# Kernel tuning notes

Measured on AMD Instinct MI355X. Metric: run time of the kernel, lower is better.

The kernel has to match this reference:

```python
import jax, jax.numpy as jnp
import numpy as np
jax.config.update("jax_enable_x64", True)

T_OLD = 60000
T_NEW = 60000
NV = 30000
MAX_STEPS = 300
FB_CHUNK = 500  # T_OLD must be divisible by this

FACE_OPP = np.array([[1, 2, 3], [0, 2, 3], [0, 1, 3], [0, 1, 2]])
EDGES = [(0, 1), (0, 2), (0, 3), (1, 2), (1, 3), (2, 3)]


def setup_inputs() -> dict:
    key = jax.random.key(0)
    k1, k2, k3, k4, k5 = jax.random.split(key, 5)
    # distinct vertices per tet (sorted base + strictly increasing offsets)
    off = jnp.arange(4, dtype=jnp.int64)
    new_indices = jnp.sort(jax.random.randint(k1, (T_NEW, 4), 0, NV - 4, dtype=jnp.int64), axis=1) + off
    old_indices = jnp.sort(jax.random.randint(k2, (T_OLD, 4), 0, NV - 4, dtype=jnp.int64), axis=1) + off
    return {
        "new_indices": new_indices,
        "old_indices": old_indices,
        "old_cc": jax.random.normal(k3, (T_OLD, 3), dtype=jnp.float32),
        "new_cc": jax.random.normal(k4, (T_NEW, 3), dtype=jnp.float32),
        "vertex_positions": jax.random.uniform(k5, (NV, 3), dtype=jnp.float32),
    }


def _min_edge_length(verts, indices):
    p = verts[indices]  # (T,4,3)
    el = jnp.stack([jnp.linalg.norm(p[:, a] - p[:, b], axis=-1) for a, b in EDGES])
    return el.min(axis=0)


def _forward(new_indices, old_indices, old_cc, new_cc, vertex_positions):
    T_new = new_indices.shape[0]
    T_old = old_indices.shape[0]
    Vn = vertex_positions.shape[0]

    # --- 1. unchanged-tet detection via sorted-vertex int64 keys ---
    key4 = lambda s: ((s[:, 0] * Vn + s[:, 1]) * Vn + s[:, 2]) * Vn + s[:, 3]
    ok = key4(jnp.sort(old_indices, axis=1))
    nk = key4(jnp.sort(new_indices, axis=1))
    order = jnp.argsort(ok)
    sk = ok[order]
    pos = jnp.searchsorted(sk, nk, side='right') - 1
    posc = jnp.clip(pos, 0, T_old - 1)
    matched = jnp.where((pos >= 0) & (sk[posc] == nk), order[posc], -1)
    is_matched = matched >= 0
    matched_safe = jnp.maximum(matched, 0)

    # --- 2. face adjacency of old mesh (sorted face keys, adjacent-equal pairing) ---
    fi = jnp.sort(old_indices[:, FACE_OPP], axis=2)          # (T_old,4,3)
    fk = (fi[..., 0] * Vn + fi[..., 1]) * Vn + fi[..., 2]    # (T_old,4)
    all_keys = fk.T.reshape(-1)                              # f-major like the numpy concat
    all_tets = jnp.tile(jnp.arange(T_old), 4)
    all_locals = jnp.repeat(jnp.arange(4), T_old)
    o2 = jnp.argsort(all_keys)
    sk2, st, sl = all_keys[o2], all_tets[o2], all_locals[o2]
    same = sk2[:-1] == sk2[1:]
    neighbors = jnp.full((T_old, 4), -1, dtype=jnp.int64)
    neighbors = neighbors.at[jnp.where(same, st[:-1], T_old), sl[:-1]].set(st[1:], mode='drop')
    neighbors = neighbors.at[jnp.where(same, st[1:], T_old), sl[1:]].set(st[:-1], mode='drop')

    # --- 3. per-old-tet inverse edge matrix; degenerate tets get no neighbors ---
    verts = jax.lax.stop_gradient(vertex_positions).astype(jnp.float32)
    p = verts[old_indices]                                   # (T_old,4,3)
    v0 = p[:, 0]
    Tm = jnp.stack([p[:, 1] - v0, p[:, 2] - v0, p[:, 3] - v0], axis=-1)
    degen = jnp.abs(jnp.linalg.det(Tm)) < 1e-10
    Tinv = jnp.linalg.inv(jnp.where(degen[:, None, None], jnp.eye(3, dtype=Tm.dtype), Tm))
    neighbors = jnp.where(degen[:, None], -1, neighbors)

    prio = jnp.full((Vn,), -1, dtype=jnp.int64)
    ar = jnp.arange(T_old)
    for vi in range(4):
        prio = prio.at[old_indices[:, vi]].max(vi * T_old + ar)
    v2t = jnp.where(prio >= 0, prio % T_old, 0)

    # --- 5. barycentric walk (masked, all float inputs stop-gradiented; int outputs) ---
    cent = jax.lax.stop_gradient(verts[new_indices].mean(axis=1))  # (T_new,3)
    seed = v2t[new_indices[:, 0]]
    n_walk = jnp.sum(~is_matched)
    thr = jnp.maximum(jnp.int64(100), n_walk // 1000)

    def cond(state):
        step, cur, rem, act = state
        return (step < MAX_STEPS) & (jnp.sum(act) >= thr)

    def body(state):
        step, cur, rem, act = state
        rel = cent - v0[cur]
        bary = jnp.einsum('nij,nj->ni', Tinv[cur], rel)
        all_b = jnp.concatenate([(1.0 - bary.sum(axis=1))[:, None], bary], axis=1)
        conv = act & (all_b.min(axis=1) >= -1e-4)
        rem = jnp.where(conv, cur, rem)
        act = act & ~conv
        nb = neighbors[cur, jnp.argmin(all_b, axis=1)]
        at_bd = act & (nb < 0)
        rem = jnp.where(at_bd, cur, rem)
        act = act & ~at_bd
        cur = jnp.where(act, nb, cur)
        return (step + 1, cur, rem, act)

    _, cur, rem, act = jax.lax.while_loop(cond, body, (jnp.int64(0), seed, seed, ~is_matched))
    rem = jnp.where(act, cur, rem)

    # --- 6. nearest-centroid fallback for unfinished walks (gated, chunked) ---
    old_cents = jax.lax.stop_gradient(verts[old_indices].mean(axis=1))

    def fallback(_):
        p2 = (cent ** 2).sum(-1)
        c2 = (old_cents ** 2).sum(-1)
        def scan_body(carry, i):
            bd, bi = carry
            c = jax.lax.dynamic_slice(old_cents, (i * FB_CHUNK, 0), (FB_CHUNK, 3))
            cn = jax.lax.dynamic_slice(c2, (i * FB_CHUNK,), (FB_CHUNK,))
            d = p2[:, None] - 2.0 * (cent @ c.T) + cn[None, :]
            md = d.min(axis=1)
            mi = d.argmin(axis=1).astype(jnp.int64) + i * FB_CHUNK
            imp = md < bd
            return (jnp.where(imp, md, bd), jnp.where(imp, mi, bi)), None
        init = (jnp.full((T_new,), jnp.inf, dtype=jnp.float32), jnp.zeros((T_new,), dtype=jnp.int64))
        (bd, bi), _ = jax.lax.scan(scan_body, init, jnp.arange(T_old // FB_CHUNK))
        return bi

    fb = jax.lax.cond(jnp.sum(act) > 0, fallback, lambda _: jnp.zeros((T_new,), dtype=jnp.int64), None)
    rem = jnp.clip(jnp.where(act, fb, rem), 0, T_old - 1)
    remap = jnp.where(is_matched, matched_safe, rem)

    # --- 7. candidates: containing tet + 4 face neighbors ---
    face_nb = neighbors[remap]
    face_nb = jnp.where(face_nb >= 0, face_nb, remap[:, None])
    cands = jnp.concatenate([remap[:, None], face_nb], axis=1)            # (T_new,5)
    cands = jnp.where(is_matched[:, None], matched_safe[:, None], cands)

    # --- 8. overlap / circumcenter-distance weights ---
    cand_verts = old_indices[cands]                                       # (T_new,5,4)
    overlap = (cand_verts[:, :, :, None] == new_indices[:, None, None, :]).any(-1).sum(-1).astype(jnp.float32)
    cc_d2 = ((old_cc[cands] - new_cc[:, None, :]) ** 2).sum(-1)
    raw = jnp.exp(overlap * 2.0) / (cc_d2 + 1e-8)
    weights = raw / raw.sum(axis=1, keepdims=True)

    # --- 9. density scale: min-edge-length ratio ---
    old_el = _min_edge_length(vertex_positions, old_indices)[cands]
    new_el = _min_edge_length(vertex_positions, new_indices)
    density_scale = jnp.clip(old_el / jnp.maximum(new_el[:, None], 1e-8), 0.1, 10.0)

    return cands, weights, density_scale


_forward_jit = jax.jit(_forward)


def reference(new_indices, old_indices, old_cc, new_cc, vertex_positions):
    return _forward_jit(new_indices, old_indices, old_cc, new_cc, vertex_positions)
```

## Files before the change

### kernel.cpp

```cpp
#include <hip/hip_runtime.h>

#pragma clang fp contract(off)

#define TOLD 60000
#define TNEW 60000
#define NVERT 30000
#define MAXSTEPS 300
#define THSZ 131072
#define FHSZ 131072
#define EMPTY64 0xFFFFFFFFFFFFFFFFULL
#define NWGR 60
#define VRANGE 500
#define NSLICE 16
#define TSLICE (TOLD / NSLICE)

#define NB_SETUP 235
#define NB_PRIO  (NWGR * NSLICE)
#define NB_NEWG  235
#define NB_FACE  938
#define NB_FOLD  118

#define OFF_TKEYS    0u
#define OFF_FTAB     1048576u
#define OFF_NBR      2097152u
#define FF_BYTES     3057152u
#define OFF_CNT      3057152u
#define OFF_TVALS    3057408u
#define OFF_PPRIO    3581696u
#define OFF_PRIO     5501696u
#define OFF_IDXOLD   5621696u
#define OFF_CUR      6581696u
#define OFF_REM      6821696u
#define OFF_DEGEN    7061696u
#define OFF_LISTA    7301696u
#define OFF_LISTB    7541696u
#define OFF_MATCHED  7781696u
#define OFF_TV4      8021696u
#define OFF_COLD4    10901696u
#define OFF_CNEW4    11861696u
#define OFF_DM       12821696u

struct P {
  const unsigned int* rawNew;
  const unsigned int* rawOld;
  const float* occ;
  const float* ncc;
  const float* verts;
  float* out;
  unsigned long long* tkeys;
  unsigned long long* ftab;
  int* counters;
  int* tvals;
  int* idxOld;
  int* nbr;
  int* pprio;
  int* prio;
  int* cur; int* rem;
  int* degen;
  int* listA; int* listB;
  int* matched;
  float4* Tv4;
  float4* cold4;
  float4* cnew4;
  unsigned int* dm;
  unsigned int dmMask;
};

__device__ __forceinline__ unsigned hash64(unsigned long long k){
  k ^= k >> 33; k *= 0xff51afd7ed558ccdULL;
  k ^= k >> 33; k *= 0xc4ceb9fe1a85ec53ULL;
  k ^= k >> 33;
  return (unsigned)k;
}
__device__ __forceinline__ void cswap(int& a, int& b){ if (a > b){ int t = a; a = b; b = t; } }

__device__ __forceinline__ int detect64(const unsigned int* raw){
  unsigned acc = 0;
  const uint4* r4 = (const uint4*)raw;
  #pragma unroll
  for (int k = 0; k < 32; ++k){ uint4 v = r4[k]; acc |= (v.y | v.w); }
  return acc == 0u;
}

__device__ __forceinline__ int4 load_tet4(const unsigned int* raw, int is64, int t){
  if (is64){
    uint4 a = ((const uint4*)raw)[t * 2 + 0];
    uint4 b = ((const uint4*)raw)[t * 2 + 1];
    return make_int4((int)a.x, (int)a.z, (int)b.x, (int)b.z);
  }
  uint4 a = ((const uint4*)raw)[t];
  return make_int4((int)a.x, (int)a.y, (int)a.z, (int)a.w);
}

__device__ __forceinline__ void face_insert(unsigned long long* ftab, int* nbr,
                                            unsigned long long fkey, int t, int l){
  unsigned long long mine = (fkey << 18) | (unsigned long long)(t * 4 + l);
  unsigned slot = hash64(fkey ^ 0x9e3779b97f4a7c15ULL) & (FHSZ - 1);
  while (true){
    unsigned long long prev = atomicCAS(&ftab[slot], EMPTY64, mine);
    if (prev == EMPTY64) return;
    if ((prev >> 18) == fkey){
      int oid = (int)(prev & 0x3FFFFULL);
      nbr[t * 4 + l] = oid >> 2;
      nbr[oid] = t;
      return;
    }
    slot = (slot + 1) & (FHSZ - 1);
  }
}

__device__ __forceinline__ float min_edge_r(
    float q0x, float q0y, float q0z, float q1x, float q1y, float q1z,
    float q2x, float q2y, float q2z, float q3x, float q3y, float q3z){
  float m = 3.402823466e+38f;
  float dx, dy, dz, d;
  dx = q0x - q1x; dy = q0y - q1y; dz = q0z - q1z; d = sqrtf((dx*dx + dy*dy) + dz*dz); m = fminf(m, d);
  dx = q0x - q2x; dy = q0y - q2y; dz = q0z - q2z; d = sqrtf((dx*dx + dy*dy) + dz*dz); m = fminf(m, d);
  dx = q0x - q3x; dy = q0y - q3y; dz = q0z - q3z; d = sqrtf((dx*dx + dy*dy) + dz*dz); m = fminf(m, d);
  dx = q1x - q2x; dy = q1y - q2y; dz = q1z - q2z; d = sqrtf((dx*dx + dy*dy) + dz*dz); m = fminf(m, d);
  dx = q1x - q3x; dy = q1y - q3y; dz = q1z - q3z; d = sqrtf((dx*dx + dy*dy) + dz*dz); m = fminf(m, d);
  dx = q2x - q3x; dy = q2y - q3y; dz = q2z - q3z; d = sqrtf((dx*dx + dy*dy) + dz*dz); m = fminf(m, d);
  return m;
}

__global__ __launch_bounds__(256) void k_front(P p){
  __shared__ int sprio[VRANGE];
  int bb = blockIdx.x;
  if (bb < NB_SETUP){
    int t = bb * 256 + threadIdx.x;
    if (bb == 0 && threadIdx.x < 64) p.counters[threadIdx.x] = 0;
    if (t >= TOLD) return;
    int is64 = detect64(p.rawOld);
    int4 iv4 = load_tet4(p.rawOld, is64, t);
    int i0 = iv4.x, i1 = iv4.y, i2 = iv4.z, i3 = iv4.w;
    ((int4*)p.idxOld)[t] = iv4;

    {
      int s0 = i0, s1 = i1, s2 = i2, s3 = i3;
      cswap(s0, s1); cswap(s2, s3); cswap(s0, s2); cswap(s1, s3); cswap(s1, s2);
      unsigned long long key =
          (unsigned long long)((((long long)s0 * NVERT + s1) * NVERT + s2) * NVERT + s3);
      unsigned slot = hash64(key) & (THSZ - 1);
      while (true){
        unsigned long long prev = atomicCAS(&p.tkeys[slot], EMPTY64, key);
        if (prev == EMPTY64 || prev == key){ atomicMax(&p.tvals[slot], t); break; }
        slot = (slot + 1) & (THSZ - 1);
      }
    }

    if (p.dmMask){
      const int FO[4][3] = {{1, 2, 3}, {0, 2, 3}, {0, 1, 3}, {0, 1, 2}};
      int iv[4] = {i0, i1, i2, i3};
      #pragma unroll
      for (int l = 0; l < 4; ++l){
        int a = iv[FO[l][0]], b = iv[FO[l][1]], c = iv[FO[l][2]];
        cswap(a, b); cswap(a, c); cswap(b, c);
        unsigned long long fk = (unsigned long long)(((long long)a * NVERT + b) * NVERT + c);
        p.dm[hash64(fk) & p.dmMask] = (unsigned)(t * 4 + l);
      }
    }

    float q0x = p.verts[i0 * 3 + 0], q0y = p.verts[i0 * 3 + 1], q0z = p.verts[i0 * 3 + 2];
    float q1x = p.verts[i1 * 3 + 0], q1y = p.verts[i1 * 3 + 1], q1z = p.verts[i1 * 3 + 2];
    float q2x = p.verts[i2 * 3 + 0], q2y = p.verts[i2 * 3 + 1], q2z = p.verts[i2 * 3 + 2];
    float q3x = p.verts[i3 * 3 + 0], q3y = p.verts[i3 * 3 + 1], q3z = p.verts[i3 * 3 + 2];
    float e1x = q1x - q0x, e1y = q1y - q0y, e1z = q1z - q0z;
    float e2x = q2x - q0x, e2y = q2y - q0y, e2z = q2z - q0z;
    float e3x = q3x - q0x, e3y = q3y - q0y, e3z = q3z - q0z;
    float c23x = e2y * e3z - e2z * e3y;
    float c23y = e2z * e3x - e2x * e3z;
    float c23z = e2x * e3y - e2y * e3x;
    float det = e1x * c23x + e1y * c23y + e1z * c23z;
    int dg = (fabsf(det) < 1e-10f) ? 1 : 0;
    p.degen[t] = dg;
    float4 r0, r1, r2;
    if (dg){
      r0 = make_float4(1.f, 0.f, 0.f, q0x);
      r1 = make_float4(0.f, 1.f, 0.f, q0y);
      r2 = make_float4(0.f, 0.f, 1.f, q0z);
    } else {
      float inv = 1.0f / det;
      float c31x = e3y * e1z - e3z * e1y;
      float c31y = e3z * e1x - e3x * e1z;
      float c31z = e3x * e1y - e3y * e1x;
      float c12x = e1y * e2z - e1z * e2y;
      float c12y = e1z * e2x - e1x * e2z;
      float c12z = e1x * e2y - e1y * e2x;
      r0 = make_float4(c23x * inv, c23y * inv, c23z * inv, q0x);
      r1 = make_float4(c31x * inv, c31y * inv, c31z * inv, q0y);
      r2 = make_float4(c12x * inv, c12y * inv, c12z * inv, q0z);
    }
    p.Tv4[t * 3 + 0] = r0;
    p.Tv4[t * 3 + 1] = r1;
    p.Tv4[t * 3 + 2] = r2;
    float el = min_edge_r(q0x, q0y, q0z, q1x, q1y, q1z, q2x, q2y, q2z, q3x, q3y, q3z);
    p.cold4[t] = make_float4((((q0x + q1x) + q2x) + q3x) * 0.25f,
                             (((q0y + q1y) + q2y) + q3y) * 0.25f,
                             (((q0z + q1z) + q2z) + q3z) * 0.25f, el);
  } else if (bb < NB_SETUP + NB_PRIO){
    int rb = bb - NB_SETUP;
    int range = rb / NSLICE;
    int slice = rb % NSLICE;
    int base = range * VRANGE;
    for (int j = threadIdx.x; j < VRANGE; j += 256) sprio[j] = -1;
    __syncthreads();
    int is64 = detect64(p.rawOld);
    int t0 = slice * TSLICE;
    for (int t = t0 + threadIdx.x; t < t0 + TSLICE; t += 256){
      int4 iv = load_tet4(p.rawOld, is64, t);
      int v;
      v = iv.x - base; if ((unsigned)v < VRANGE) atomicMax(&sprio[v], 0 * TOLD + t);
      v = iv.y - base; if ((unsigned)v < VRANGE) atomicMax(&sprio[v], 1 * TOLD + t);
      v = iv.z - base; if ((unsigned)v < VRANGE) atomicMax(&sprio[v], 2 * TOLD + t);
      v = iv.w - base; if ((unsigned)v < VRANGE) atomicMax(&sprio[v], 3 * TOLD + t);
    }
    __syncthreads();
    for (int j = threadIdx.x; j < VRANGE; j += 256)
      p.pprio[slice * NVERT + base + j] = sprio[j];
  } else {
    int n = (bb - NB_SETUP - NB_PRIO) * 256 + threadIdx.x;
    if (n >= TNEW) return;
    int is64 = detect64(p.rawNew);
    int4 ni = load_tet4(p.rawNew, is64, n);
    float q0x = p.verts[ni.x * 3 + 0], q0y = p.verts[ni.x * 3 + 1], q0z = p.verts[ni.x * 3 + 2];
    float q1x = p.verts[ni.y * 3 + 0], q1y = p.verts[ni.y * 3 + 1], q1z = p.verts[ni.y * 3 + 2];
    float q2x = p.verts[ni.z * 3 + 0], q2y = p.verts[ni.z * 3 + 1], q2z = p.verts[ni.z * 3 + 2];
    float q3x = p.verts[ni.w * 3 + 0], q3y = p.verts[ni.w * 3 + 1], q3z = p.verts[ni.w * 3 + 2];
    float el = min_edge_r(q0x, q0y, q0z, q1x, q1y, q1z, q2x, q2y, q2z, q3x, q3y, q3z);
    p.cnew4[n] = make_float4((((q0x + q1x) + q2x) + q3x) * 0.25f,
                             (((q0y + q1y) + q2y) + q3y) * 0.25f,
                             (((q0z + q1z) + q2z) + q3z) * 0.25f, el);
  }
}

__global__ __launch_bounds__(256) void k_mid(P p){
  int bb = blockIdx.x;
  if (bb < NB_FACE){
    int i = bb * 256 + threadIdx.x;
    if (i >= TOLD * 4) return;
    int t = i >> 2, l = i & 3;
    int4 iv4 = ((const int4*)p.idxOld)[t];
    int iv[4] = {iv4.x, iv4.y, iv4.z, iv4.w};
    const int FO[4][3] = {{1, 2, 3}, {0, 2, 3}, {0, 1, 3}, {0, 1, 2}};
    int a = iv[FO[l][0]], b = iv[FO[l][1]], c = iv[FO[l][2]];
    cswap(a, b); cswap(a, c); cswap(b, c);
    unsigned long long fk = (unsigned long long)(((long long)a * NVERT + b) * NVERT + c);
    if (p.dmMask){
      unsigned wid = p.dm[hash64(fk) & p.dmMask];
      if (wid == (unsigned)i) return;
      if (wid < (unsigned)(TOLD * 4)){
        int wt = wid >> 2, wl = (int)(wid & 3u);
        int4 wv4 = ((const int4*)p.idxOld)[wt];
        int wv[4] = {wv4.x, wv4.y, wv4.z, wv4.w};
        int wa = wv[FO[wl][0]], wb = wv[FO[wl][1]], wc = wv[FO[wl][2]];
        cswap(wa, wb); cswap(wa, wc); cswap(wb, wc);
        unsigned long long wfk = (unsigned long long)(((long long)wa * NVERT + wb) * NVERT + wc);
        if (wfk == fk){
          p.nbr[i] = wt;
          p.nbr[wid] = t;
          return;
        }
      }
    }
    face_insert(p.ftab, p.nbr, fk, t, l);
  } else {
    int v = (bb - NB_FACE) * 256 + threadIdx.x;
    if (v >= NVERT) return;
    int pr = -1;
    #pragma unroll
    for (int s = 0; s < NSLICE; ++s) pr = max(pr, p.pprio[s * NVERT + v]);
    p.prio[v] = pr;
  }
}

__device__ __forceinline__ bool walk_step(const P& p, int n){
  int c = p.cur[n];
  float4 r0 = p.Tv4[c * 3 + 0];
  float4 r1 = p.Tv4[c * 3 + 1];
  float4 r2 = p.Tv4[c * 3 + 2];
  float4 cn = p.cnew4[n];
  float rx = cn.x - r0.w, ry = cn.y - r1.w, rz = cn.z - r2.w;
  float b0 = r0.x * rx + r0.y * ry + r0.z * rz;
  float b1 = r1.x * rx + r1.y * ry + r1.z * rz;
  float b2 = r2.x * rx + r2.y * ry + r2.z * rz;
  float a0 = 1.0f - (b0 + b1 + b2);
  float ab[4] = {a0, b0, b1, b2};
  int amin = 0; float mn = ab[0];
  for (int j = 1; j < 4; ++j){ if (ab[j] < mn){ mn = ab[j]; amin = j; } }
  if (mn >= -0.0001f){ p.rem[n] = c; return false; }
  int nb = p.degen[c] ? -1 : p.nbr[c * 4 + amin];
  if (nb < 0){ p.rem[n] = c; return false; }
  p.cur[n] = nb;
  return true;
}

__global__ __launch_bounds__(256) void k_new2(P p){
  int n = blockIdx.x * blockDim.x + threadIdx.x;
  if (n >= TNEW) return;
  int is64 = detect64(p.rawNew);
  int4 ni = load_tet4(p.rawNew, is64, n);
  int s0 = ni.x, s1 = ni.y, s2 = ni.z, s3 = ni.w;
  cswap(s0, s1); cswap(s2, s3); cswap(s0, s2); cswap(s1, s3); cswap(s1, s2);
  unsigned long long key =
      (unsigned long long)((((long long)s0 * NVERT + s1) * NVERT + s2) * NVERT + s3);
  int m = -1;
  {
    unsigned slot = hash64(key) & (THSZ - 1);
    while (true){
      unsigned long long k = p.tkeys[slot];
      if (k == EMPTY64) break;
      if (k == key){ m = p.tvals[slot]; break; }
      slot = (slot + 1) & (THSZ - 1);
    }
  }
  p.matched[n] = m;
  if (m >= 0) return;
  int pr = p.prio[ni.x];
  int seed = (pr >= 0) ? (pr % TOLD) : 0;
  p.cur[n] = seed;
  p.rem[n] = seed;
  p.listB[atomicAdd(&p.counters[0], 1)] = n;
  if (walk_step(p, n))
    p.listA[atomicAdd(&p.counters[1], 1)] = n;
}

__global__ void __launch_bounds__(1024) k_persist(P p){
  __shared__ int s_cnt;
  int nw = p.counters[0];
  if (nw < 100){
    if (threadIdx.x == 0){ p.counters[4] = nw; p.counters[5] = 1; }
    return;
  }
  int thr = max(100, nw / 1000);
  if (threadIdx.x == 0) s_cnt = atomicAdd(&p.counters[1], 0);
  __syncthreads();
  int count = s_cnt;
  int use_a = 1;
  int step = 1;
  while (step < MAXSTEPS && count >= thr){
    int* curL = use_a ? p.listA : p.listB;
    int* nxtL = use_a ? p.listB : p.listA;
    int* nxtC = use_a ? &p.counters[2] : &p.counters[1];
    int* curC = use_a ? &p.counters[1] : &p.counters[2];
    for (int i = threadIdx.x; i < count; i += blockDim.x){
      int n = curL[i];
      if (walk_step(p, n)){
        int pos = atomicAdd(nxtC, 1);
        nxtL[pos] = n;
      }
    }
    __syncthreads();
    if (threadIdx.x == 0){
      s_cnt = atomicAdd(nxtC, 0);
      atomicExch(curC, 0);
    }
    __syncthreads();
    count = s_cnt;
    use_a ^= 1;
    ++step;
  }
  if (threadIdx.x == 0){
    p.counters[4] = count;
    p.counters[5] = use_a ? 0 : 1;
  }
}

__global__ __launch_bounds__(256) void k_fallback(P p){
  __shared__ float sd[256];
  __shared__ int si[256];
  int fc = p.counters[4];
  const int* lst = p.counters[5] ? p.listB : p.listA;
  for (int e = blockIdx.x; e < fc; e += gridDim.x){
    int n = lst[e];
    float4 cn = p.cnew4[n];
    float cx = cn.x, cy = cn.y, cz = cn.z;
    float p2 = (cx * cx + cy * cy) + cz * cz;
    float bd = 3.402823466e+38f; int bi = 0;
    for (int j = threadIdx.x; j < TOLD; j += 256){
      float4 oc = p.cold4[j];
      float dot = (cx * oc.x + cy * oc.y) + cz * oc.z;
      float c2 = (oc.x * oc.x + oc.y * oc.y) + oc.z * oc.z;
      float d = (p2 - 2.0f * dot) + c2;
      if (d < bd || (d == bd && j < bi)){ bd = d; bi = j; }
    }
    sd[threadIdx.x] = bd; si[threadIdx.x] = bi;
    __syncthreads();
    for (int s = 128; s > 0; s >>= 1){
      if ((int)threadIdx.x < s){
        float od = sd[threadIdx.x + s]; int oi = si[threadIdx.x + s];
        if (od < sd[threadIdx.x] || (od == sd[threadIdx.x] && oi < si[threadIdx.x])){
          sd[threadIdx.x] = od; si[threadIdx.x] = oi;
        }
      }
      __syncthreads();
    }
    if (threadIdx.x == 0){
      int r = si[0];
      if (r < 0) r = 0; if (r > TOLD - 1) r = TOLD - 1;
      p.rem[n] = r;
    }
    __syncthreads();
  }
}

__global__ __launch_bounds__(256) void k_assemble(P p){
  int n = blockIdx.x * blockDim.x + threadIdx.x;
  if (n >= TNEW) return;
  int m = p.matched[n];
  int remap = (m >= 0) ? m : p.rem[n];
  int cds[5];
  cds[0] = remap;
  int dg = p.degen[remap];
  int4 nb4 = ((const int4*)p.nbr)[remap];
  int nbl[4] = {nb4.x, nb4.y, nb4.z, nb4.w};
  for (int l = 0; l < 4; ++l){
    int fb = dg ? -1 : nbl[l];
    cds[1 + l] = (fb >= 0) ? fb : remap;
  }
  if (m >= 0){ for (int c = 0; c < 5; ++c) cds[c] = m; }
  int is64 = detect64(p.rawNew);
  int4 ni = load_tet4(p.rawNew, is64, n);
  float nc0 = p.ncc[n * 3 + 0], nc1 = p.ncc[n * 3 + 1], nc2 = p.ncc[n * 3 + 2];
  float raws[5]; float rsum = 0.0f;
  float oels[5];
  for (int c = 0; c < 5; ++c){
    int ct = cds[c];
    int4 cv = ((const int4*)p.idxOld)[ct];
    int ov = 0;
    ov += (cv.x == ni.x || cv.x == ni.y || cv.x == ni.z || cv.x == ni.w) ? 1 : 0;
    ov += (cv.y == ni.x || cv.y == ni.y || cv.y == ni.z || cv.y == ni.w) ? 1 : 0;
    ov += (cv.z == ni.x || cv.z == ni.y || cv.z == ni.z || cv.z == ni.w) ? 1 : 0;
    ov += (cv.w == ni.x || cv.w == ni.y || cv.w == ni.z || cv.w == ni.w) ? 1 : 0;
    float d0 = p.occ[ct * 3 + 0] - nc0;
    float d1 = p.occ[ct * 3 + 1] - nc1;
    float d2 = p.occ[ct * 3 + 2] - nc2;
    float ccd2 = (d0 * d0 + d1 * d1) + d2 * d2;
    float raw = expf((float)ov * 2.0f) / (ccd2 + 1e-8f);
    raws[c] = raw; rsum += raw;
    oels[c] = p.cold4[ct].w;
  }
  float nelv = fmaxf(p.cnew4[n].w, 1e-8f);
  for (int c = 0; c < 5; ++c){
    p.out[n * 5 + c] = (float)cds[c];
    p.out[TNEW * 5 + n * 5 + c] = raws[c] / rsum;
    float ds = oels[c] / nelv;
    ds = fminf(fmaxf(ds, 0.1f), 10.0f);
    p.out[2 * TNEW * 5 + n * 5 + c] = ds;
  }
}

extern "C" void kernel_launch(void* const* d_in, const int* in_sizes, int n_in,
                              void* d_out, int out_size, void* d_ws, size_t ws_size,
                              hipStream_t stream) {
  char* w = (char*)d_ws;
  P p;
  p.rawNew = (const unsigned int*)d_in[0];
  p.rawOld = (const unsigned int*)d_in[1];
  p.occ    = (const float*)d_in[2];
  p.ncc    = (const float*)d_in[3];
  p.verts  = (const float*)d_in[4];
  p.out    = (float*)d_out;
  p.tkeys    = (unsigned long long*)(w + OFF_TKEYS);
  p.ftab     = (unsigned long long*)(w + OFF_FTAB);
  p.nbr      = (int*)(w + OFF_NBR);
  p.counters = (int*)(w + OFF_CNT);
  p.tvals    = (int*)(w + OFF_TVALS);
  p.pprio    = (int*)(w + OFF_PPRIO);
  p.prio     = (int*)(w + OFF_PRIO);
  p.idxOld   = (int*)(w + OFF_IDXOLD);
  p.cur      = (int*)(w + OFF_CUR);
  p.rem      = (int*)(w + OFF_REM);
  p.degen    = (int*)(w + OFF_DEGEN);
  p.listA    = (int*)(w + OFF_LISTA);
  p.listB    = (int*)(w + OFF_LISTB);
  p.matched  = (int*)(w + OFF_MATCHED);
  p.Tv4      = (float4*)(w + OFF_TV4);
  p.cold4    = (float4*)(w + OFF_COLD4);
  p.cnew4    = (float4*)(w + OFF_CNEW4);
  p.dm       = (unsigned int*)(w + OFF_DM);
  size_t avail = (ws_size > (size_t)OFF_DM) ? ws_size - (size_t)OFF_DM : 0;
  unsigned dmMask = 0;
  for (int bshift = 21; bshift >= 16; --bshift){
    if (avail >= ((size_t)4 << bshift)){ dmMask = (1u << bshift) - 1u; break; }
  }
  p.dmMask = dmMask;

  hipMemsetAsync(w, 0xFF, FF_BYTES, stream);
  hipLaunchKernelGGL(k_front,    dim3(NB_SETUP + NB_PRIO + NB_NEWG), dim3(256), 0, stream, p);
  hipLaunchKernelGGL(k_mid,      dim3(NB_FACE + NB_FOLD), dim3(256), 0, stream, p);
  hipLaunchKernelGGL(k_new2,     dim3((TNEW + 255) / 256), dim3(256), 0, stream, p);
  hipLaunchKernelGGL(k_persist,  dim3(1), dim3(1024), 0, stream, p);
  hipLaunchKernelGGL(k_fallback, dim3(120), dim3(256), 0, stream, p);
  hipLaunchKernelGGL(k_assemble, dim3((TNEW + 255) / 256), dim3(256), 0, stream, p);
}
```

Measured before the change: 130.6 us.

## Fuse fallback and assembly kernels, move match lookup into mid kernel

Moves the unchanged-tet hash lookup into the face-adjacency kernel as extra blocks, so the walker-init kernel only reads the match flag and one vertex. Merges the brute-force nearest-circumcenter fallback and the output assembly into one kernel: fallback walkers are marked with rem=-1 and assembled by the fallback block's lead thread, and all others are assembled in parallel blocks. It also adds a fast path when all five candidates are identical and replaces the atomicMax on a fresh hash-slot insert with a plain store. This removes one kernel launch and a dependency boundary. In exchange, fallback assembly now runs on a single thread per block.

```diff
diff --git a/kernel.cpp b/kernel.cpp
--- a/kernel.cpp
+++ b/kernel.cpp
@@ -19,6 +19,9 @@
 #define NB_NEWG  235
 #define NB_FACE  938
 #define NB_FOLD  118
+#define NB_MATCH 235
+#define NB_FB    120
+#define NB_ASM   235
 
 #define OFF_TKEYS    0u
 #define OFF_FTAB     1048576u
@@ -143,7 +146,8 @@
       unsigned slot = hash64(key) & (THSZ - 1);
       while (true){
         unsigned long long prev = atomicCAS(&p.tkeys[slot], EMPTY64, key);
-        if (prev == EMPTY64 || prev == key){ atomicMax(&p.tvals[slot], t); break; }
+        if (prev == EMPTY64){ p.tvals[slot] = t; break; }
+        if (prev == key){ atomicMax(&p.tvals[slot], t); break; }
         slot = (slot + 1) & (THSZ - 1);
       }
     }
@@ -263,13 +267,31 @@
       }
     }
     face_insert(p.ftab, p.nbr, fk, t, l);
-  } else {
+  } else if (bb < NB_FACE + NB_FOLD){
     int v = (bb - NB_FACE) * 256 + threadIdx.x;
     if (v >= NVERT) return;
     int pr = -1;
     #pragma unroll
     for (int s = 0; s < NSLICE; ++s) pr = max(pr, p.pprio[s * NVERT + v]);
     p.prio[v] = pr;
+  } else {
+    int n = (bb - NB_FACE - NB_FOLD) * 256 + threadIdx.x;
+    if (n >= TNEW) return;
+    int is64 = detect64(p.rawNew);
+    int4 ni = load_tet4(p.rawNew, is64, n);
+    int s0 = ni.x, s1 = ni.y, s2 = ni.z, s3 = ni.w;
+    cswap(s0, s1); cswap(s2, s3); cswap(s0, s2); cswap(s1, s3); cswap(s1, s2);
+    unsigned long long key =
+        (unsigned long long)((((long long)s0 * NVERT + s1) * NVERT + s2) * NVERT + s3);
+    int m = -1;
+    unsigned slot = hash64(key) & (THSZ - 1);
+    while (true){
+      unsigned long long k = p.tkeys[slot];
+      if (k == EMPTY64) break;
+      if (k == key){ m = p.tvals[slot]; break; }
+      slot = (slot + 1) & (THSZ - 1);
+    }
+    p.matched[n] = m;
   }
 }
 
@@ -294,28 +316,13 @@
   return true;
 }
 
-__global__ __launch_bounds__(256) void k_new2(P p){
+__global__ __launch_bounds__(256) void k_new3(P p){
   int n = blockIdx.x * blockDim.x + threadIdx.x;
   if (n >= TNEW) return;
+  if (p.matched[n] >= 0) return;
   int is64 = detect64(p.rawNew);
-  int4 ni = load_tet4(p.rawNew, is64, n);
-  int s0 = ni.x, s1 = ni.y, s2 = ni.z, s3 = ni.w;
-  cswap(s0, s1); cswap(s2, s3); cswap(s0, s2); cswap(s1, s3); cswap(s1, s2);
-  unsigned long long key =
-      (unsigned long long)((((long long)s0 * NVERT + s1) * NVERT + s2) * NVERT + s3);
-  int m = -1;
-  {
-    unsigned slot = hash64(key) & (THSZ - 1);
-    while (true){
-      unsigned long long k = p.tkeys[slot];
-      if (k == EMPTY64) break;
-      if (k == key){ m = p.tvals[slot]; break; }
-      slot = (slot + 1) & (THSZ - 1);
-    }
-  }
-  p.matched[n] = m;
-  if (m >= 0) return;
-  int pr = p.prio[ni.x];
+  int i0 = is64 ? (int)((const long long*)p.rawNew)[n * 4] : ((const int*)p.rawNew)[n * 4];
+  int pr = p.prio[i0];
   int seed = (pr >= 0) ? (pr % TOLD) : 0;
   p.cur[n] = seed;
   p.rem[n] = seed;
@@ -328,6 +335,7 @@
   __shared__ int s_cnt;
   int nw = p.counters[0];
   if (nw < 100){
+    for (int i = threadIdx.x; i < nw; i += blockDim.x) p.rem[p.listB[i]] = -1;
     if (threadIdx.x == 0){ p.counters[4] = nw; p.counters[5] = 1; }
     return;
   }
@@ -359,68 +367,60 @@
     use_a ^= 1;
     ++step;
   }
+  const int* fl = use_a ? p.listA : p.listB;
+  for (int i = threadIdx.x; i < count; i += blockDim.x) p.rem[fl[i]] = -1;
   if (threadIdx.x == 0){
     p.counters[4] = count;
     p.counters[5] = use_a ? 0 : 1;
   }
 }
 
-__global__ __launch_bounds__(256) void k_fallback(P p){
-  __shared__ float sd[256];
-  __shared__ int si[256];
-  int fc = p.counters[4];
-  const int* lst = p.counters[5] ? p.listB : p.listA;
-  for (int e = blockIdx.x; e < fc; e += gridDim.x){
-    int n = lst[e];
-    float4 cn = p.cnew4[n];
-    float cx = cn.x, cy = cn.y, cz = cn.z;
-    float p2 = (cx * cx + cy * cy) + cz * cz;
-    float bd = 3.402823466e+38f; int bi = 0;
-    for (int j = threadIdx.x; j < TOLD; j += 256){
-      float4 oc = p.cold4[j];
-      float dot = (cx * oc.x + cy * oc.y) + cz * oc.z;
-      float c2 = (oc.x * oc.x + oc.y * oc.y) + oc.z * oc.z;
-      float d = (p2 - 2.0f * dot) + c2;
-      if (d < bd || (d == bd && j < bi)){ bd = d; bi = j; }
-    }
-    sd[threadIdx.x] = bd; si[threadIdx.x] = bi;
-    __syncthreads();
-    for (int s = 128; s > 0; s >>= 1){
-      if ((int)threadIdx.x < s){
-        float od = sd[threadIdx.x + s]; int oi = si[threadIdx.x + s];
-        if (od < sd[threadIdx.x] || (od == sd[threadIdx.x] && oi < si[threadIdx.x])){
-          sd[threadIdx.x] = od; si[threadIdx.x] = oi;
-        }
-      }
-      __syncthreads();
-    }
-    if (threadIdx.x == 0){
-      int r = si[0];
-      if (r < 0) r = 0; if (r > TOLD - 1) r = TOLD - 1;
-      p.rem[n] = r;
-    }
-    __syncthreads();
-  }
-}
-
-__global__ __launch_bounds__(256) void k_assemble(P p){
-  int n = blockIdx.x * blockDim.x + threadIdx.x;
-  if (n >= TNEW) return;
-  int m = p.matched[n];
-  int remap = (m >= 0) ? m : p.rem[n];
+__device__ __forceinline__ void assemble_walker(const P& p, int n, int m, int remap){
   int cds[5];
-  cds[0] = remap;
-  int dg = p.degen[remap];
-  int4 nb4 = ((const int4*)p.nbr)[remap];
-  int nbl[4] = {nb4.x, nb4.y, nb4.z, nb4.w};
-  for (int l = 0; l < 4; ++l){
-    int fb = dg ? -1 : nbl[l];
-    cds[1 + l] = (fb >= 0) ? fb : remap;
-  }
-  if (m >= 0){ for (int c = 0; c < 5; ++c) cds[c] = m; }
+  if (m >= 0){
+    cds[0] = cds[1] = cds[2] = cds[3] = cds[4] = m;
+  } else {
+    cds[0] = remap;
+    int dg = p.degen[remap];
+    int4 nb4 = ((const int4*)p.nbr)[remap];
+    int nbl[4] = {nb4.x, nb4.y, nb4.z, nb4.w};
+    for (int l = 0; l < 4; ++l){
+      int fb = dg ? -1 : nbl[l];
+      cds[1 + l] = (fb >= 0) ? fb : remap;
+    }
+  }
+  bool same = (cds[1] == cds[0]) & (cds[2] == cds[0]) &
+              (cds[3] == cds[0]) & (cds[4] == cds[0]);
   int is64 = detect64(p.rawNew);
   int4 ni = load_tet4(p.rawNew, is64, n);
   float nc0 = p.ncc[n * 3 + 0], nc1 = p.ncc[n * 3 + 1], nc2 = p.ncc[n * 3 + 2];
+  float nelv = fmaxf(p.cnew4[n].w, 1e-8f);
+  if (same){
+    int ct = cds[0];
+    int4 cv = ((const int4*)p.idxOld)[ct];
+    int ov = 0;
+    ov += (cv.x == ni.x || cv.x == ni.y || cv.x == ni.z || cv.x == ni.w) ? 1 : 0;
+    ov += (cv.y == ni.x || cv.y == ni.y || cv.y == ni.z || cv.y == ni.w) ? 1 : 0;
+    ov += (cv.z == ni.x || cv.z == ni.y || cv.z == ni.z || cv.z == ni.w) ? 1 : 0;
+    ov += (cv.w == ni.x || cv.w == ni.y || cv.w == ni.z || cv.w == ni.w) ? 1 : 0;
+    float d0 = p.occ[ct * 3 + 0] - nc0;
+    float d1 = p.occ[ct * 3 + 1] - nc1;
+    float d2 = p.occ[ct * 3 + 2] - nc2;
+    float ccd2 = (d0 * d0 + d1 * d1) + d2 * d2;
+    float raw = expf((float)ov * 2.0f) / (ccd2 + 1e-8f);
+    float rsum = 0.0f;
+    rsum += raw; rsum += raw; rsum += raw; rsum += raw; rsum += raw;
+    float wgt = raw / rsum;
+    float ds = p.cold4[ct].w / nelv;
+    ds = fminf(fmaxf(ds, 0.1f), 10.0f);
+    float cf = (float)ct;
+    for (int c = 0; c < 5; ++c){
+      p.out[n * 5 + c] = cf;
+      p.out[TNEW * 5 + n * 5 + c] = wgt;
+      p.out[2 * TNEW * 5 + n * 5 + c] = ds;
+    }
+    return;
+  }
   float raws[5]; float rsum = 0.0f;
   float oels[5];
   for (int c = 0; c < 5; ++c){
@@ -439,13 +439,63 @@
     raws[c] = raw; rsum += raw;
     oels[c] = p.cold4[ct].w;
   }
-  float nelv = fmaxf(p.cnew4[n].w, 1e-8f);
   for (int c = 0; c < 5; ++c){
     p.out[n * 5 + c] = (float)cds[c];
     p.out[TNEW * 5 + n * 5 + c] = raws[c] / rsum;
     float ds = oels[c] / nelv;
     ds = fminf(fmaxf(ds, 0.1f), 10.0f);
     p.out[2 * TNEW * 5 + n * 5 + c] = ds;
+  }
+}
+
+__global__ __launch_bounds__(256) void k_tail(P p){
+  __shared__ float sd[256];
+  __shared__ int si[256];
+  int bb = blockIdx.x;
+  if (bb < NB_FB){
+    int fc = p.counters[4];
+    const int* lst = p.counters[5] ? p.listB : p.listA;
+    for (int e = bb; e < fc; e += NB_FB){
+      int n = lst[e];
+      float4 cn = p.cnew4[n];
+      float cx = cn.x, cy = cn.y, cz = cn.z;
+      float p2 = (cx * cx + cy * cy) + cz * cz;
+      float bd = 3.402823466e+38f; int bi = 0;
+      for (int j = threadIdx.x; j < TOLD; j += 256){
+        float4 oc = p.cold4[j];
+        float dot = (cx * oc.x + cy * oc.y) + cz * oc.z;
+        float c2 = (oc.x * oc.x + oc.y * oc.y) + oc.z * oc.z;
+        float d = (p2 - 2.0f * dot) + c2;
+        if (d < bd || (d == bd && j < bi)){ bd = d; bi = j; }
+      }
+      sd[threadIdx.x] = bd; si[threadIdx.x] = bi;
+      __syncthreads();
+      for (int s = 128; s > 0; s >>= 1){
+        if ((int)threadIdx.x < s){
+          float od = sd[threadIdx.x + s]; int oi = si[threadIdx.x + s];
+          if (od < sd[threadIdx.x] || (od == sd[threadIdx.x] && oi < si[threadIdx.x])){
+            sd[threadIdx.x] = od; si[threadIdx.x] = oi;
+          }
+        }
+        __syncthreads();
+      }
+      if (threadIdx.x == 0){
+        int r = si[0];
+        if (r < 0) r = 0; if (r > TOLD - 1) r = TOLD - 1;
+        assemble_walker(p, n, -1, r);
+      }
+      __syncthreads();
+    }
+  } else {
+    int n = (bb - NB_FB) * 256 + threadIdx.x;
+    if (n >= TNEW) return;
+    int m = p.matched[n];
+    int remap = 0;
+    if (m < 0){
+      remap = p.rem[n];
+      if (remap < 0) return;
+    }
+    assemble_walker(p, n, m, remap);
   }
 }
 
@@ -486,10 +536,9 @@
   p.dmMask = dmMask;
 
   hipMemsetAsync(w, 0xFF, FF_BYTES, stream);
-  hipLaunchKernelGGL(k_front,    dim3(NB_SETUP + NB_PRIO + NB_NEWG), dim3(256), 0, stream, p);
-  hipLaunchKernelGGL(k_mid,      dim3(NB_FACE + NB_FOLD), dim3(256), 0, stream, p);
-  hipLaunchKernelGGL(k_new2,     dim3((TNEW + 255) / 256), dim3(256), 0, stream, p);
-  hipLaunchKernelGGL(k_persist,  dim3(1), dim3(1024), 0, stream, p);
-  hipLaunchKernelGGL(k_fallback, dim3(120), dim3(256), 0, stream, p);
-  hipLaunchKernelGGL(k_assemble, dim3((TNEW + 255) / 256), dim3(256), 0, stream, p);
-}
+  hipLaunchKernelGGL(k_front,   dim3(NB_SETUP + NB_PRIO + NB_NEWG), dim3(256), 0, stream, p);
+  hipLaunchKernelGGL(k_mid,     dim3(NB_FACE + NB_FOLD + NB_MATCH), dim3(256), 0, stream, p);
+  hipLaunchKernelGGL(k_new3,    dim3((TNEW + 255) / 256), dim3(256), 0, stream, p);
+  hipLaunchKernelGGL(k_persist, dim3(1), dim3(1024), 0, stream, p);
+  hipLaunchKernelGGL(k_tail,    dim3(NB_FB + NB_ASM), dim3(256), 0, stream, p);
+}
```

Measured after the change: 123.9 us. 1.05x faster.
